# Kernel tuning notes

Measured on AMD Instinct MI355X. Metric: run time of the kernel, lower is better.

The kernel has to match this reference:

```python
import jax, jax.numpy as jnp
import numpy as np

SAI, B, CK, H, W = 9, 4, 64, 32, 32
CV = 64
RADIUS = 4.0 / 8.0  # valid_dis_range / 8


def setup_inputs() -> dict:
    key = jax.random.key(0)
    k1, k2, k3, k4, k5 = jax.random.split(key, 5)
    return {
        "memory_keys": jax.random.normal(k1, (SAI, B, CK, H, W), dtype=jnp.float32),
        "memory_values": jax.random.normal(k2, (SAI, B, CV, H, W), dtype=jnp.float32),
        "query_query": jax.random.normal(k3, (B, CK, H, W), dtype=jnp.float32),
        "disparity": jax.random.normal(k4, (B, 1, H, W), dtype=jnp.float32),
        "sequence_index": jax.random.randint(k5, (B, SAI, 2), 0, 11, dtype=jnp.int32),
    }


def reference(memory_keys, memory_values, query_query, disparity, sequence_index):
    sai, b, ck, h, w = memory_keys.shape
    cv = memory_values.shape[2]
    shw = sai * h * w

    # keys: (sai,b,ck,h,w) -> (b, ck, sai*h*w)
    keys = jnp.transpose(memory_keys, (1, 2, 0, 3, 4)).reshape(b, ck, shw)
    # query: (b, ck, h*w) -> (b, h*w, ck)
    q = query_query.reshape(b, ck, h * w).transpose(0, 2, 1)
    # scores: (b, h*w, sai*h*w)
    scores = jnp.einsum("bqc,bck->bqk", q, keys)

    # distance-based additive mask (per batch, per frame, per key pixel)
    seq = sequence_index.astype(jnp.float32)
    dist = jnp.sqrt((seq[:, :, 1] - 5.0) ** 2 + (seq[:, :, 0] - 5.0) ** 2)  # (b, sai)
    # total_disparity: (b, sai, h, w); disparity is (b,1,h,w)
    total = dist[:, :, None, None] * disparity
    large = jnp.abs(total) > RADIUS  # mask==1 where |disp| exceeds radius
    # bias: 0 where mask==1, -inf where mask==0 (per original masked_fill)
    bias = jnp.where(large, 0.0, -jnp.inf).reshape(b, 1, shw)

    scores = scores + bias  # broadcasts over query positions
    attn = jax.nn.softmax(scores, axis=-1)

    # values: (sai,b,cv,h,w) -> (b, sai*h*w, cv)
    vals = jnp.transpose(memory_values, (1, 2, 0, 3, 4)).reshape(b, cv, shw).transpose(0, 2, 1)
    mem = jnp.einsum("bqk,bkc->bqc", attn, vals)  # (b, h*w, cv)
    return mem.transpose(0, 2, 1).reshape(b, cv, h, w)
```

## Files before the change

kernel.cpp:

```cpp
#include <hip/hip_runtime.h>
#include <math.h>

#define SAI 9
#define NB  4
#define CK  64
#define CV  64
#define HW  1024
#define RSW 136
#define RSTR 68

typedef __attribute__((ext_vector_type(8))) short bf16x8;
typedef __attribute__((ext_vector_type(4))) float f32x4;
typedef unsigned short u16;
typedef unsigned int u32;

__device__ __forceinline__ u16 f2bf(float x) {
    unsigned u = __float_as_uint(x);
    return (u16)((u + 0x7fff + ((u >> 16) & 1)) >> 16);
}
__device__ __forceinline__ float bf2f(u16 s) {
    return __uint_as_float(((unsigned)s) << 16);
}
__device__ __forceinline__ unsigned pk2(float a, float b) {
    return (unsigned)f2bf(a) | ((unsigned)f2bf(b) << 16);
}

__global__ __launch_bounds__(256) void cfa_prep(
    const float* __restrict__ keys, const float* __restrict__ vals,
    u16* __restrict__ khi, u16* __restrict__ klo, u16* __restrict__ vbf)
{
    const int gid = blockIdx.x * 256 + threadIdx.x;
    const int isV = gid >= (SAI * NB * 8192);
    const int id  = isV ? gid - SAI * NB * 8192 : gid;
    const int f   = id >> 13;
    const int r   = id & 8191;
    const int lane = r & 63;
    const int gg   = r >> 6;
    const int l15 = lane & 15, quad = lane >> 4;
    const size_t fb = (size_t)f * (64 * 1024);

    if (!isV) {
        const int p  = (gg >> 1) * 16 + l15;
        const int c0 = (gg & 1) * 32 + quad * 8;
        const float* src = keys + fb + (size_t)c0 * HW + p;
        float x[8];
#pragma unroll
        for (int j = 0; j < 8; ++j) x[j] = src[(size_t)j * HW];
        uint4 ph, pl;
        u32* php = (u32*)&ph; u32* plp = (u32*)&pl;
#pragma unroll
        for (int h2 = 0; h2 < 4; ++h2) {
            u16 h0 = f2bf(x[h2 * 2]),     h1 = f2bf(x[h2 * 2 + 1]);
            u16 l0 = f2bf(x[h2 * 2] - bf2f(h0));
            u16 l1 = f2bf(x[h2 * 2 + 1] - bf2f(h1));
            php[h2] = (u32)h0 | ((u32)h1 << 16);
            plp[h2] = (u32)l0 | ((u32)l1 << 16);
        }
        const size_t dst = fb + (size_t)gg * 512 + lane * 8;
        *(uint4*)&khi[dst] = ph;
        *(uint4*)&klo[dst] = pl;
    } else {
        const int p = (gg >> 2) * 32 + quad * 8;
        const int c = (gg & 3) * 16 + l15;
        const float* src = vals + fb + (size_t)c * HW + p;
        const float4 a = *(const float4*)src;
        const float4 b = *(const float4*)(src + 4);
        uint4 pv;
        pv.x = pk2(a.x, a.y); pv.y = pk2(a.z, a.w);
        pv.z = pk2(b.x, b.y); pv.w = pk2(b.z, b.w);
        *(uint4*)&vbf[fb + (size_t)gg * 512 + lane * 8] = pv;
    }
}

__global__ __launch_bounds__(256, 4) void cfa_main(
    const u16* __restrict__ khi, const u16* __restrict__ klo,
    const u16* __restrict__ vbf,
    const float* __restrict__ query, const float* __restrict__ disp,
    const int* __restrict__ seq,
    float* __restrict__ numW, float* __restrict__ denW)
{
    __shared__ alignas(16) u16 sW[32 * RSW];
    __shared__ float sDen[4 * 32];

    const int tid = threadIdx.x;
    const int w = tid >> 6;
    const int lane = tid & 63;
    const int l15 = lane & 15, quad = lane >> 4;
    const int qt = blockIdx.x;
    const int b  = blockIdx.y;
    const int s  = blockIdx.z;
    const int p0 = qt * 32;
    const int f  = s * NB + b;
    const size_t fb = (size_t)f * (64 * 1024);

    const float d0 = (float)seq[(b * SAI + s) * 2 + 0] - 5.f;
    const float d1 = (float)seq[(b * SAI + s) * 2 + 1] - 5.f;
    const float dist = sqrtf(d0 * d0 + d1 * d1);

    bf16x8 qh[2][2], ql[2][2];
#pragma unroll
    for (int q2 = 0; q2 < 2; ++q2)
#pragma unroll
        for (int ks = 0; ks < 2; ++ks)
#pragma unroll
            for (int j = 0; j < 8; ++j) {
                float x = query[(size_t)(b * CK + ks * 32 + quad * 8 + j) * HW + p0 + q2 * 16 + l15];
                u16 h = f2bf(x);
                qh[q2][ks][j] = (short)h;
                ql[q2][ks][j] = (short)f2bf(x - bf2f(h));
            }

    f32x4 acc[2];
#pragma unroll
    for (int q2 = 0; q2 < 2; ++q2)
#pragma unroll
        for (int r = 0; r < 4; ++r) acc[q2][r] = 0.f;
    float den[2] = {0.f, 0.f};

    for (int t = 0; t < 8; ++t) {
        __syncthreads();

        f32x4 sc[2][2];
#pragma unroll
        for (int q2 = 0; q2 < 2; ++q2)
#pragma unroll
            for (int kt = 0; kt < 2; ++kt)
#pragma unroll
                for (int r = 0; r < 4; ++r) sc[q2][kt][r] = 0.f;

#pragma unroll
        for (int kt = 0; kt < 2; ++kt) {
            const int g16 = t * 8 + w * 2 + kt;
#pragma unroll
            for (int ks = 0; ks < 2; ++ks) {
                const size_t ka = fb + (size_t)(g16 * 2 + ks) * 512 + lane * 8;
                const bf16x8 kh = __builtin_bit_cast(bf16x8, *(const uint4*)&khi[ka]);
                const bf16x8 kl = __builtin_bit_cast(bf16x8, *(const uint4*)&klo[ka]);
#pragma unroll
                for (int q2 = 0; q2 < 2; ++q2) {
                    sc[q2][kt] = __builtin_amdgcn_mfma_f32_16x16x32_bf16(kh, qh[q2][ks], sc[q2][kt], 0, 0, 0);
                    sc[q2][kt] = __builtin_amdgcn_mfma_f32_16x16x32_bf16(kl, qh[q2][ks], sc[q2][kt], 0, 0, 0);
                    sc[q2][kt] = __builtin_amdgcn_mfma_f32_16x16x32_bf16(kh, ql[q2][ks], sc[q2][kt], 0, 0, 0);
                }
            }
        }

#pragma unroll
        for (int kt = 0; kt < 2; ++kt) {
            const int kb = t * 128 + w * 32 + kt * 16 + quad * 4;
            const float4 dv = *(const float4*)(disp + b * HW + kb);
            const float m0 = (fabsf(dist * dv.x) > 0.5f) ? 1.f : 0.f;
            const float m1 = (fabsf(dist * dv.y) > 0.5f) ? 1.f : 0.f;
            const float m2 = (fabsf(dist * dv.z) > 0.5f) ? 1.f : 0.f;
            const float m3 = (fabsf(dist * dv.w) > 0.5f) ? 1.f : 0.f;
#pragma unroll
            for (int q2 = 0; q2 < 2; ++q2) {
                const float e0 = m0 * __expf(sc[q2][kt][0]);
                const float e1 = m1 * __expf(sc[q2][kt][1]);
                const float e2 = m2 * __expf(sc[q2][kt][2]);
                const float e3 = m3 * __expf(sc[q2][kt][3]);
                den[q2] += (e0 + e1) + (e2 + e3);
                uint2 pk;
                pk.x = pk2(e0, e1);
                pk.y = pk2(e2, e3);
                *(uint2*)&sW[(q2 * 16 + l15) * RSW + w * 32 + kt * 16 + quad * 4] = pk;
            }
        }
        __syncthreads();

#pragma unroll
        for (int k2 = 0; k2 < 4; ++k2) {
            const size_t va = fb + (size_t)((t * 4 + k2) * 4 + w) * 512 + lane * 8;
            const bf16x8 vf = __builtin_bit_cast(bf16x8, *(const uint4*)&vbf[va]);
#pragma unroll
            for (int q2 = 0; q2 < 2; ++q2) {
                const bf16x8 wf = __builtin_bit_cast(bf16x8,
                    *(const uint4*)&sW[(q2 * 16 + l15) * RSW + k2 * 32 + quad * 8]);
                acc[q2] = __builtin_amdgcn_mfma_f32_16x16x32_bf16(wf, vf, acc[q2], 0, 0, 0);
            }
        }
    }

#pragma unroll
    for (int q2 = 0; q2 < 2; ++q2) {
        den[q2] += __shfl_xor(den[q2], 16, 64);
        den[q2] += __shfl_xor(den[q2], 32, 64);
    }
    if (quad == 0) {
#pragma unroll
        for (int q2 = 0; q2 < 2; ++q2)
            sDen[w * 32 + q2 * 16 + l15] = den[q2];
    }
    __syncthreads();
    if (tid < 32)
        denW[(size_t)f * HW + p0 + tid] =
            sDen[tid] + sDen[32 + tid] + sDen[64 + tid] + sDen[96 + tid];

#pragma unroll
    for (int q2 = 0; q2 < 2; ++q2)
#pragma unroll
        for (int r = 0; r < 4; ++r) {
            const int q = q2 * 16 + quad * 4 + r;
            const int c = w * 16 + l15;
            numW[((size_t)f * HW + p0 + q) * CV + c] = acc[q2][r];
        }
}

__global__ __launch_bounds__(256) void cfa_reduce(
    const float* __restrict__ numW, const float* __restrict__ denW,
    float* __restrict__ out)
{
    const int tid = threadIdx.x;
    const int bid = blockIdx.x;
    const int b = bid >> 8;
    const int p = (bid & 255) * 4 + (tid >> 6);
    const int c = tid & 63;
    float num = 0.f, den = 0.f;
#pragma unroll
    for (int s = 0; s < SAI; ++s) {
        num += numW[(((size_t)(s * NB + b)) * HW + p) * CV + c];
        den += denW[((size_t)(s * NB + b)) * HW + p];
    }
    out[((size_t)b * CV + c) * HW + p] = num / den;
}

__global__ __launch_bounds__(256, 2) void cfa_fb(
    const float* __restrict__ keys, const float* __restrict__ vals,
    const float* __restrict__ query, const float* __restrict__ disp,
    const int* __restrict__ seq,
    float* __restrict__ numW, float* __restrict__ denW,
    float* __restrict__ out, int nS)
{
    __shared__ alignas(16) unsigned int sV[CV * RSTR];
    __shared__ alignas(16) unsigned int sWb[32 * RSTR];
    __shared__ float sDen[4 * 32];
    __shared__ float sDenTot[32];

    const int tid  = threadIdx.x;
    const int w    = tid >> 6;
    const int lane = tid & 63;
    const int l15  = lane & 15;
    const int quad = lane >> 4;
    const int b    = blockIdx.y;
    const int s0   = blockIdx.z;
    const int p0   = blockIdx.x * 32;
    const bool direct = (nS == SAI);

    bf16x8 qhi[2][2], qlo[2][2];
#pragma unroll
    for (int qt = 0; qt < 2; ++qt)
#pragma unroll
        for (int ks = 0; ks < 2; ++ks)
#pragma unroll
            for (int j = 0; j < 8; ++j) {
                float x = query[(size_t)(b * CK + ks * 32 + quad * 8 + j) * HW + p0 + qt * 16 + l15];
                u16 h = f2bf(x);
                qhi[qt][ks][j] = (short)h;
                qlo[qt][ks][j] = (short)f2bf(x - bf2f(h));
            }

    f32x4 acc[2];
#pragma unroll
    for (int qt = 0; qt < 2; ++qt)
#pragma unroll
        for (int r = 0; r < 4; ++r) acc[qt][r] = 0.f;
    float denacc[2][4] = {{0.f,0.f,0.f,0.f},{0.f,0.f,0.f,0.f}};

    for (int si = 0; si < nS; ++si) {
        const int s = s0 + si;
        const float d0 = (float)seq[(b * SAI + s) * 2 + 0] - 5.f;
        const float d1 = (float)seq[(b * SAI + s) * 2 + 1] - 5.f;
        const float dist = sqrtf(d0 * d0 + d1 * d1);
        const float* Kf = keys + (size_t)(s * NB + b) * CK * HW;
        const float* Vf = vals + (size_t)(s * NB + b) * CV * HW;

        for (int t = 0; t < HW / 128; ++t) {
            const int t128 = t * 128;
            __syncthreads();
#pragma unroll
            for (int it = 0; it < 4; ++it) {
                const int gidx = it * 256 + tid;
                const int c = gidx >> 4;
                const int g = gidx & 15;
                const float* vp = Vf + (size_t)c * HW + t128 + g * 8;
                const float4 f0 = *(const float4*)(vp);
                const float4 f1 = *(const float4*)(vp + 4);
                uint4 pk;
                pk.x = pk2(f0.x, f0.y); pk.y = pk2(f0.z, f0.w);
                pk.z = pk2(f1.x, f1.y); pk.w = pk2(f1.z, f1.w);
                *(uint4*)&sV[c * RSTR + g * 4] = pk;
            }

            f32x4 sc[2][2];
#pragma unroll
            for (int qt = 0; qt < 2; ++qt)
#pragma unroll
                for (int kt = 0; kt < 2; ++kt)
#pragma unroll
                    for (int r = 0; r < 4; ++r) sc[qt][kt][r] = 0.f;

            const int keyBase = t128 + w * 32 + l15;
#pragma unroll
            for (int kt = 0; kt < 2; ++kt)
#pragma unroll
                for (int ks = 0; ks < 2; ++ks) {
                    bf16x8 kh, kl;
#pragma unroll
                    for (int j = 0; j < 8; ++j) {
                        float x = Kf[(size_t)(ks * 32 + quad * 8 + j) * HW + keyBase + kt * 16];
                        u16 h = f2bf(x);
                        kh[j] = (short)h;
                        kl[j] = (short)f2bf(x - bf2f(h));
                    }
#pragma unroll
                    for (int qt = 0; qt < 2; ++qt) {
                        sc[qt][kt] = __builtin_amdgcn_mfma_f32_16x16x32_bf16(qhi[qt][ks], kh, sc[qt][kt], 0, 0, 0);
                        sc[qt][kt] = __builtin_amdgcn_mfma_f32_16x16x32_bf16(qhi[qt][ks], kl, sc[qt][kt], 0, 0, 0);
                        sc[qt][kt] = __builtin_amdgcn_mfma_f32_16x16x32_bf16(qlo[qt][ks], kh, sc[qt][kt], 0, 0, 0);
                    }
                }

#pragma unroll
            for (int kt = 0; kt < 2; ++kt) {
                const int kk = w * 32 + kt * 16 + l15;
                const float dv = disp[b * HW + t128 + kk];
                const float msk = (fabsf(dist * dv) > 0.5f) ? 1.f : 0.f;
#pragma unroll
                for (int qt = 0; qt < 2; ++qt)
#pragma unroll
                    for (int r = 0; r < 4; ++r) {
                        const float e = msk * __expf(sc[qt][kt][r]);
                        denacc[qt][r] += e;
                        const int q = qt * 16 + quad * 4 + r;
                        ((u16*)sWb)[q * (2 * RSTR) + kk] = f2bf(e);
                    }
            }
            __syncthreads();

            const int c = w * 16 + l15;
#pragma unroll
            for (int ks2 = 0; ks2 < 4; ++ks2) {
                const int g = ks2 * 4 + quad;
                uint4 vr = *(uint4*)&sV[c * RSTR + g * 4];
                bf16x8 vfrag = __builtin_bit_cast(bf16x8, vr);
#pragma unroll
                for (int qt = 0; qt < 2; ++qt) {
                    const int q = qt * 16 + l15;
                    uint4 wr = *(uint4*)&sWb[q * RSTR + g * 4];
                    bf16x8 wfrag = __builtin_bit_cast(bf16x8, wr);
                    acc[qt] = __builtin_amdgcn_mfma_f32_16x16x32_bf16(wfrag, vfrag, acc[qt], 0, 0, 0);
                }
            }
        }
    }

#pragma unroll
    for (int off = 1; off < 16; off <<= 1)
#pragma unroll
        for (int qt = 0; qt < 2; ++qt)
#pragma unroll
            for (int r = 0; r < 4; ++r)
                denacc[qt][r] += __shfl_xor(denacc[qt][r], off, 64);

    if (l15 == 0)
#pragma unroll
        for (int qt = 0; qt < 2; ++qt)
#pragma unroll
            for (int r = 0; r < 4; ++r)
                sDen[w * 32 + qt * 16 + quad * 4 + r] = denacc[qt][r];
    __syncthreads();

    if (tid < 32) {
        const float d = sDen[tid] + sDen[32 + tid] + sDen[64 + tid] + sDen[96 + tid];
        if (direct) sDenTot[tid] = d;
        else        denW[(size_t)(s0 * NB + b) * HW + p0 + tid] = d;
    }

    if (direct) {
        __syncthreads();
#pragma unroll
        for (int qt = 0; qt < 2; ++qt)
#pragma unroll
            for (int r = 0; r < 4; ++r) {
                const int q = qt * 16 + quad * 4 + r;
                const int c = w * 16 + l15;
                out[((size_t)b * CV + c) * HW + p0 + q] = acc[qt][r] / sDenTot[q];
            }
    } else {
#pragma unroll
        for (int qt = 0; qt < 2; ++qt)
#pragma unroll
            for (int r = 0; r < 4; ++r) {
                const int q = qt * 16 + quad * 4 + r;
                const int c = w * 16 + l15;
                numW[((size_t)(s0 * NB + b) * HW + p0 + q) * CV + c] = acc[qt][r];
            }
    }
}

extern "C" void kernel_launch(void* const* d_in, const int* in_sizes, int n_in,
                              void* d_out, int out_size, void* d_ws, size_t ws_size,
                              hipStream_t stream) {
    const float* keys  = (const float*)d_in[0];
    const float* vals  = (const float*)d_in[1];
    const float* query = (const float*)d_in[2];
    const float* disp  = (const float*)d_in[3];
    const int*   seq   = (const int*)d_in[4];
    float* out = (float*)d_out;

    const size_t numElems = (size_t)SAI * NB * HW * CV;
    const size_t denElems = (size_t)SAI * NB * HW;
    const size_t partBytes = (numElems + denElems) * sizeof(float);
    const size_t fragBytes = (size_t)SAI * NB * CK * HW * 2;
    const size_t needFull = partBytes + 3 * fragBytes;

    float* numW = (float*)d_ws;
    float* denW = numW + numElems;

    if (ws_size >= needFull) {
        u16* khi = (u16*)((char*)d_ws + partBytes);
        u16* klo = (u16*)((char*)khi + fragBytes);
        u16* vbf = (u16*)((char*)klo + fragBytes);
        hipLaunchKernelGGL(cfa_prep, dim3(2 * SAI * NB * 8192 / 256), dim3(256), 0, stream,
                           keys, vals, khi, klo, vbf);
        hipLaunchKernelGGL(cfa_main, dim3(HW / 32, NB, SAI), dim3(256), 0, stream,
                           khi, klo, vbf, query, disp, seq, numW, denW);
        hipLaunchKernelGGL(cfa_reduce, dim3(1024), dim3(256), 0, stream,
                           numW, denW, out);
    } else if (ws_size >= partBytes) {
        hipLaunchKernelGGL(cfa_fb, dim3(HW / 32, NB, SAI), dim3(256), 0, stream,
                           keys, vals, query, disp, seq, numW, denW, (float*)nullptr, 1);
        hipLaunchKernelGGL(cfa_reduce, dim3(1024), dim3(256), 0, stream,
                           numW, denW, out);
    } else {
        hipLaunchKernelGGL(cfa_fb, dim3(HW / 32, NB, 1), dim3(256), 0, stream,
                           keys, vals, query, disp, seq,
                           (float*)nullptr, (float*)nullptr, out, SAI);
    }
}
```

Baseline: 120.7 us.

## Give each wave private key slice and reduce partial outputs in LDS

Each wave now handles its own 32-key slice for the P·V product across all 64 value channels, keeping its exp-weights in a private LDS region. This removes the two block-wide barriers per key tile. The partial outputs from the four waves are combined at the end through a two-step LDS tree reduction. The trade-off is four times the accumulator registers, lower launch-bounds occupancy (3 instead of 4 blocks), extra LDS for the reduction buffers, and a serialized reduction tail.

```diff
diff --git a/kernel.cpp b/kernel.cpp
--- a/kernel.cpp
+++ b/kernel.cpp
@@ -6,7 +6,8 @@
 #define CK  64
 #define CV  64
 #define HW  1024
-#define RSW 136
+#define WST 40
+#define RST 68
 #define RSTR 68
 
 typedef __attribute__((ext_vector_type(8))) short bf16x8;
@@ -72,15 +73,16 @@
     }
 }
 
-__global__ __launch_bounds__(256, 4) void cfa_main(
+__global__ __launch_bounds__(256, 3) void cfa_main(
     const u16* __restrict__ khi, const u16* __restrict__ klo,
     const u16* __restrict__ vbf,
     const float* __restrict__ query, const float* __restrict__ disp,
     const int* __restrict__ seq,
     float* __restrict__ numW, float* __restrict__ denW)
 {
-    __shared__ alignas(16) u16 sW[32 * RSW];
-    __shared__ float sDen[4 * 32];
+    __shared__ alignas(16) u16 sW[4 * 32 * WST];
+    __shared__ alignas(16) float sRed[2][32 * RST];
+    __shared__ float sDen[128];
 
     const int tid = threadIdx.x;
     const int w = tid >> 6;
@@ -110,16 +112,18 @@
                 ql[q2][ks][j] = (short)f2bf(x - bf2f(h));
             }
 
-    f32x4 acc[2];
+    f32x4 acc[2][4];
 #pragma unroll
     for (int q2 = 0; q2 < 2; ++q2)
 #pragma unroll
-        for (int r = 0; r < 4; ++r) acc[q2][r] = 0.f;
+        for (int cg = 0; cg < 4; ++cg)
+#pragma unroll
+            for (int r = 0; r < 4; ++r) acc[q2][cg][r] = 0.f;
     float den[2] = {0.f, 0.f};
 
+    u16* const myW = &sW[w * 32 * WST];
+
     for (int t = 0; t < 8; ++t) {
-        __syncthreads();
-
         f32x4 sc[2][2];
 #pragma unroll
         for (int q2 = 0; q2 < 2; ++q2)
@@ -163,21 +167,22 @@
                 uint2 pk;
                 pk.x = pk2(e0, e1);
                 pk.y = pk2(e2, e3);
-                *(uint2*)&sW[(q2 * 16 + l15) * RSW + w * 32 + kt * 16 + quad * 4] = pk;
+                *(uint2*)&myW[(q2 * 16 + l15) * WST + kt * 16 + quad * 4] = pk;
             }
         }
-        __syncthreads();
-
-#pragma unroll
-        for (int k2 = 0; k2 < 4; ++k2) {
-            const size_t va = fb + (size_t)((t * 4 + k2) * 4 + w) * 512 + lane * 8;
+
+        bf16x8 wf[2];
+#pragma unroll
+        for (int q2 = 0; q2 < 2; ++q2)
+            wf[q2] = __builtin_bit_cast(bf16x8,
+                *(const uint4*)&myW[(q2 * 16 + l15) * WST + quad * 8]);
+#pragma unroll
+        for (int cg = 0; cg < 4; ++cg) {
+            const size_t va = fb + (size_t)((t * 4 + w) * 4 + cg) * 512 + lane * 8;
             const bf16x8 vf = __builtin_bit_cast(bf16x8, *(const uint4*)&vbf[va]);
 #pragma unroll
-            for (int q2 = 0; q2 < 2; ++q2) {
-                const bf16x8 wf = __builtin_bit_cast(bf16x8,
-                    *(const uint4*)&sW[(q2 * 16 + l15) * RSW + k2 * 32 + quad * 8]);
-                acc[q2] = __builtin_amdgcn_mfma_f32_16x16x32_bf16(wf, vf, acc[q2], 0, 0, 0);
-            }
+            for (int q2 = 0; q2 < 2; ++q2)
+                acc[q2][cg] = __builtin_amdgcn_mfma_f32_16x16x32_bf16(wf[q2], vf, acc[q2][cg], 0, 0, 0);
         }
     }
 
@@ -191,19 +196,60 @@
         for (int q2 = 0; q2 < 2; ++q2)
             sDen[w * 32 + q2 * 16 + l15] = den[q2];
     }
+
     __syncthreads();
+
     if (tid < 32)
         denW[(size_t)f * HW + p0 + tid] =
             sDen[tid] + sDen[32 + tid] + sDen[64 + tid] + sDen[96 + tid];
 
-#pragma unroll
-    for (int q2 = 0; q2 < 2; ++q2)
-#pragma unroll
-        for (int r = 0; r < 4; ++r) {
-            const int q = q2 * 16 + quad * 4 + r;
-            const int c = w * 16 + l15;
-            numW[((size_t)f * HW + p0 + q) * CV + c] = acc[q2][r];
-        }
+    if (w >= 2) {
+        float* dst = sRed[w - 2];
+#pragma unroll
+        for (int q2 = 0; q2 < 2; ++q2)
+#pragma unroll
+            for (int cg = 0; cg < 4; ++cg)
+#pragma unroll
+                for (int r = 0; r < 4; ++r)
+                    dst[(q2 * 16 + quad * 4 + r) * RST + cg * 16 + l15] = acc[q2][cg][r];
+    }
+    __syncthreads();
+    if (w < 2) {
+        const float* srcb = sRed[w];
+#pragma unroll
+        for (int q2 = 0; q2 < 2; ++q2)
+#pragma unroll
+            for (int cg = 0; cg < 4; ++cg)
+#pragma unroll
+                for (int r = 0; r < 4; ++r)
+                    acc[q2][cg][r] += srcb[(q2 * 16 + quad * 4 + r) * RST + cg * 16 + l15];
+    }
+    if (w == 1) {
+        float* dst = sRed[1];
+#pragma unroll
+        for (int q2 = 0; q2 < 2; ++q2)
+#pragma unroll
+            for (int cg = 0; cg < 4; ++cg)
+#pragma unroll
+                for (int r = 0; r < 4; ++r)
+                    dst[(q2 * 16 + quad * 4 + r) * RST + cg * 16 + l15] = acc[q2][cg][r];
+    }
+    __syncthreads();
+    if (w == 0) {
+        const float* srcb = sRed[1];
+#pragma unroll
+        for (int q2 = 0; q2 < 2; ++q2)
+#pragma unroll
+            for (int r = 0; r < 4; ++r) {
+                const int q = q2 * 16 + quad * 4 + r;
+#pragma unroll
+                for (int cg = 0; cg < 4; ++cg) {
+                    const int c = cg * 16 + l15;
+                    numW[((size_t)f * HW + p0 + q) * CV + c] =
+                        acc[q2][cg][r] + srcb[q * RST + c];
+                }
+            }
+    }
 }
 
 __global__ __launch_bounds__(256) void cfa_reduce(
```

Measured after the change: 135.0 us. +11.9%, slower.

## Software-pipeline key loads and double-buffer LDS weights in main attention kernel

Applied to the files above, without the earlier changes.

Prefetches the next tile's key fragments into registers during the current tile. Values and disparity are loaded at the start of each iteration. The softmax-weight LDS buffer is double-buffered, which removes one of the two block barriers per iteration; the remaining one becomes a waitcnt plus s_barrier. Together these are meant to hide global-load latency behind MFMA work. In exchange, register pressure rises, so the occupancy hint drops from 4 to 3 blocks, which could reduce latency hiding elsewhere.

```diff
diff --git a/kernel.cpp b/kernel.cpp
--- a/kernel.cpp
+++ b/kernel.cpp
@@ -6,6 +6,7 @@
 #define CK  64
 #define CV  64
 #define HW  1024
+#define QT  32
 #define RSW 136
 #define RSTR 68
 
@@ -23,6 +24,9 @@
 }
 __device__ __forceinline__ unsigned pk2(float a, float b) {
     return (unsigned)f2bf(a) | ((unsigned)f2bf(b) << 16);
+}
+__device__ __forceinline__ void lds_barrier() {
+    __asm__ __volatile__("s_waitcnt lgkmcnt(0)\n\ts_barrier" ::: "memory");
 }
 
 __global__ __launch_bounds__(256) void cfa_prep(
@@ -72,24 +76,23 @@
     }
 }
 
-__global__ __launch_bounds__(256, 4) void cfa_main(
+__global__ __launch_bounds__(256, 3) void cfa_main(
     const u16* __restrict__ khi, const u16* __restrict__ klo,
     const u16* __restrict__ vbf,
     const float* __restrict__ query, const float* __restrict__ disp,
     const int* __restrict__ seq,
     float* __restrict__ numW, float* __restrict__ denW)
 {
-    __shared__ alignas(16) u16 sW[32 * RSW];
-    __shared__ float sDen[4 * 32];
+    __shared__ alignas(16) u16 sW[2][QT * RSW];
+    __shared__ float sDen[4 * QT];
 
     const int tid = threadIdx.x;
     const int w = tid >> 6;
     const int lane = tid & 63;
     const int l15 = lane & 15, quad = lane >> 4;
-    const int qt = blockIdx.x;
     const int b  = blockIdx.y;
     const int s  = blockIdx.z;
-    const int p0 = qt * 32;
+    const int p0 = blockIdx.x * QT;
     const int f  = s * NB + b;
     const size_t fb = (size_t)f * (64 * 1024);
 
@@ -117,8 +120,29 @@
         for (int r = 0; r < 4; ++r) acc[q2][r] = 0.f;
     float den[2] = {0.f, 0.f};
 
+    uint4 kbh[2][2], kbl[2][2];
+#define LOADK(tt)                                                              \
+    {                                                                          \
+        _Pragma("unroll") for (int kt = 0; kt < 2; ++kt)                       \
+        _Pragma("unroll") for (int ks = 0; ks < 2; ++ks) {                     \
+            const size_t ka = fb +                                             \
+                (size_t)((((tt) * 8 + w * 2 + kt) * 2) + ks) * 512 + lane * 8; \
+            kbh[kt][ks] = *(const uint4*)&khi[ka];                             \
+            kbl[kt][ks] = *(const uint4*)&klo[ka];                             \
+        }                                                                      \
+    }
+
+    LOADK(0);
+
     for (int t = 0; t < 8; ++t) {
-        __syncthreads();
+        u16* const wbuf = sW[t & 1];
+
+        uint4 vb[4];
+#pragma unroll
+        for (int k2 = 0; k2 < 4; ++k2)
+            vb[k2] = *(const uint4*)&vbf[fb + (size_t)((t * 4 + k2) * 4 + w) * 512 + lane * 8];
+        const float4 dv0 = *(const float4*)(disp + b * HW + t * 128 + w * 32 + quad * 4);
+        const float4 dv1 = *(const float4*)(disp + b * HW + t * 128 + w * 32 + 16 + quad * 4);
 
         f32x4 sc[2][2];
 #pragma unroll
@@ -129,13 +153,11 @@
                 for (int r = 0; r < 4; ++r) sc[q2][kt][r] = 0.f;
 
 #pragma unroll
-        for (int kt = 0; kt < 2; ++kt) {
-            const int g16 = t * 8 + w * 2 + kt;
+        for (int kt = 0; kt < 2; ++kt)
 #pragma unroll
             for (int ks = 0; ks < 2; ++ks) {
-                const size_t ka = fb + (size_t)(g16 * 2 + ks) * 512 + lane * 8;
-                const bf16x8 kh = __builtin_bit_cast(bf16x8, *(const uint4*)&khi[ka]);
-                const bf16x8 kl = __builtin_bit_cast(bf16x8, *(const uint4*)&klo[ka]);
+                const bf16x8 kh = __builtin_bit_cast(bf16x8, kbh[kt][ks]);
+                const bf16x8 kl = __builtin_bit_cast(bf16x8, kbl[kt][ks]);
 #pragma unroll
                 for (int q2 = 0; q2 < 2; ++q2) {
                     sc[q2][kt] = __builtin_amdgcn_mfma_f32_16x16x32_bf16(kh, qh[q2][ks], sc[q2][kt], 0, 0, 0);
@@ -143,12 +165,10 @@
                     sc[q2][kt] = __builtin_amdgcn_mfma_f32_16x16x32_bf16(kh, ql[q2][ks], sc[q2][kt], 0, 0, 0);
                 }
             }
-        }
 
 #pragma unroll
         for (int kt = 0; kt < 2; ++kt) {
-            const int kb = t * 128 + w * 32 + kt * 16 + quad * 4;
-            const float4 dv = *(const float4*)(disp + b * HW + kb);
+            const float4 dv = kt ? dv1 : dv0;
             const float m0 = (fabsf(dist * dv.x) > 0.5f) ? 1.f : 0.f;
             const float m1 = (fabsf(dist * dv.y) > 0.5f) ? 1.f : 0.f;
             const float m2 = (fabsf(dist * dv.z) > 0.5f) ? 1.f : 0.f;
@@ -163,23 +183,26 @@
                 uint2 pk;
                 pk.x = pk2(e0, e1);
                 pk.y = pk2(e2, e3);
-                *(uint2*)&sW[(q2 * 16 + l15) * RSW + w * 32 + kt * 16 + quad * 4] = pk;
+                *(uint2*)&wbuf[(q2 * 16 + l15) * RSW + w * 32 + kt * 16 + quad * 4] = pk;
             }
         }
-        __syncthreads();
+
+        LOADK((t + 1) & 7);
+
+        lds_barrier();
 
 #pragma unroll
         for (int k2 = 0; k2 < 4; ++k2) {
-            const size_t va = fb + (size_t)((t * 4 + k2) * 4 + w) * 512 + lane * 8;
-            const bf16x8 vf = __builtin_bit_cast(bf16x8, *(const uint4*)&vbf[va]);
+            const bf16x8 vf = __builtin_bit_cast(bf16x8, vb[k2]);
 #pragma unroll
             for (int q2 = 0; q2 < 2; ++q2) {
                 const bf16x8 wf = __builtin_bit_cast(bf16x8,
-                    *(const uint4*)&sW[(q2 * 16 + l15) * RSW + k2 * 32 + quad * 8]);
+                    *(const uint4*)&wbuf[(q2 * 16 + l15) * RSW + k2 * 32 + quad * 8]);
                 acc[q2] = __builtin_amdgcn_mfma_f32_16x16x32_bf16(wf, vf, acc[q2], 0, 0, 0);
             }
         }
     }
+#undef LOADK
 
 #pragma unroll
     for (int q2 = 0; q2 < 2; ++q2) {
@@ -189,12 +212,12 @@
     if (quad == 0) {
 #pragma unroll
         for (int q2 = 0; q2 < 2; ++q2)
-            sDen[w * 32 + q2 * 16 + l15] = den[q2];
+            sDen[w * QT + q2 * 16 + l15] = den[q2];
     }
     __syncthreads();
-    if (tid < 32)
+    if (tid < QT)
         denW[(size_t)f * HW + p0 + tid] =
-            sDen[tid] + sDen[32 + tid] + sDen[64 + tid] + sDen[96 + tid];
+            sDen[tid] + sDen[QT + tid] + sDen[2 * QT + tid] + sDen[3 * QT + tid];
 
 #pragma unroll
     for (int q2 = 0; q2 < 2; ++q2)
@@ -323,8 +346,8 @@
 #pragma unroll
             for (int kt = 0; kt < 2; ++kt) {
                 const int kk = w * 32 + kt * 16 + l15;
-                const float dv = disp[b * HW + t128 + kk];
-                const float msk = (fabsf(dist * dv) > 0.5f) ? 1.f : 0.f;
+                const float dvv = disp[b * HW + t128 + kk];
+                const float msk = (fabsf(dist * dvv) > 0.5f) ? 1.f : 0.f;
 #pragma unroll
                 for (int qt = 0; qt < 2; ++qt)
 #pragma unroll
@@ -423,7 +446,7 @@
         u16* vbf = (u16*)((char*)klo + fragBytes);
         hipLaunchKernelGGL(cfa_prep, dim3(2 * SAI * NB * 8192 / 256), dim3(256), 0, stream,
                            keys, vals, khi, klo, vbf);
-        hipLaunchKernelGGL(cfa_main, dim3(HW / 32, NB, SAI), dim3(256), 0, stream,
+        hipLaunchKernelGGL(cfa_main, dim3(HW / QT, NB, SAI), dim3(256), 0, stream,
                            khi, klo, vbf, query, disp, seq, numW, denW);
         hipLaunchKernelGGL(cfa_reduce, dim3(1024), dim3(256), 0, stream,
                            numW, denW, out);
```

New measurement: 114.4 us. 5.2% less time.
